# Kernel tuning notes

Measured on AMD Instinct MI355X. Metric: run time of the kernel, lower is better.

The kernel has to match this reference:

```python
import jax, jax.numpy as jnp
import numpy as np

TOPK = 2


def _conv2d(x, w, b):
    # x: (B, Cin, H, W), w: (Cout, Cin, 3, 3), SAME padding (padding=1)
    y = jax.lax.conv_general_dilated(
        x, w, window_strides=(1, 1), padding='SAME',
        dimension_numbers=('NCHW', 'OIHW', 'NCHW'))
    return y + b[None, :, None, None]


def _msunit(x2d, c1w, c1b, c2w, c2b):
    # TimesNet-style 2D unit: conv(1->d_model) -> GELU -> conv(d_model->1)
    h = jax.nn.gelu(_conv2d(x2d, c1w, c1b))
    return _conv2d(h, c2w, c2b)


def setup_inputs():
    B, T, H, DM = 256, 2048, 720, 64
    key = jax.random.key(0)
    ks = jax.random.split(key, 5)
    x = jax.random.normal(ks[0], (B, 1, T), jnp.float32)
    conv1_w = jax.random.normal(ks[1], (DM, 1, 3, 3), jnp.float32) * 0.1
    conv1_b = jnp.zeros((DM,), jnp.float32)
    conv2_w = jax.random.normal(ks[2], (1, DM, 3, 3), jnp.float32) * 0.1
    conv2_b = jnp.zeros((1,), jnp.float32)
    head_w = jax.random.normal(ks[3], (H, T), jnp.float32) * 0.02
    head_b = jnp.zeros((H,), jnp.float32)
    return {'x': x, 'conv1_w': conv1_w, 'conv1_b': conv1_b,
            'conv2_w': conv2_w, 'conv2_b': conv2_b,
            'head_w': head_w, 'head_b': head_b}


def reference(x, conv1_w, conv1_b, conv2_w, conv2_b, head_w, head_b):
    B, _, T = x.shape
    # FFT amplitude spectrum, batch-averaged, drop DC bin
    amp = jnp.abs(jnp.fft.rfft(x[:, 0, :], axis=-1)).mean(0)[1:]
    vals, idx = jax.lax.top_k(amp, TOPK)
    # data-dependent period selection (mirrors .item() calls in torch -> Python ints)
    freqs = np.asarray(idx) + 1
    P_list = [max(1, int(round(T / int(f)))) for f in freqs]
    weights = jax.nn.softmax(vals.astype(x.dtype))
    y = jnp.zeros_like(x)
    for i, P in enumerate(P_list):
        cols = (T + P - 1) // P
        pad = P * cols - T
        xp = jnp.pad(x, ((0, 0), (0, 0), (0, pad)))
        x2d = xp.reshape(B, 1, cols, P).transpose(0, 1, 3, 2)  # (B,1,P,cols)
        y2d = _msunit(x2d, conv1_w, conv1_b, conv2_w, conv2_b)  # (B,1,P,cols)
        y1d = y2d.transpose(0, 1, 3, 2).reshape(B, 1, cols * P)[..., :T]
        y = y + weights[i] * y1d
    out = y[:, 0, :] @ head_w.T + head_b  # (B, horizon)
    return out
```

## Files before the change

### kernel.cpp

```cpp
#include <hip/hip_runtime.h>
#include <math.h>

#define T_LEN   2048
#define NB      256
#define N_FREQ  1024
#define DMODEL  64
#define HORIZON 720

#define WS_META 0
#define WS_AMP  64
#define WS_Y0   2048
#define WS_Y1   (2048 + NB * T_LEN)

#define PMAX_FAST 191
#define CHUNK   1024
#define NCHUNK  2
#define HSTRIDE 1412
#define ZSLOT   1408
#define XSMAX   1824
#define ZXS     (XSMAX - 1)

typedef _Float16 h4 __attribute__((ext_vector_type(4)));
typedef float    fx4 __attribute__((ext_vector_type(4)));

__device__ __forceinline__ float gelu_fast(float a) {
    float a2 = a * a;
    float z  = a * fmaf(-0.07135481627159498f, a2, -1.5957691216057308f);
    float e  = __expf(z);
    return a * __builtin_amdgcn_rcpf(1.0f + e);
}

__device__ __forceinline__ float2 cmul(float2 a, float2 b) {
    return make_float2(a.x * b.x - a.y * b.y, a.x * b.y + a.y * b.x);
}

__device__ __forceinline__ void compute_meta(const float* __restrict__ amp,
                                             float* sf, int* si, int tid,
                                             int& P1, int& cols1, int& P2, int& cols2,
                                             float& wg1, float& wg2) {
    float* v1s = sf;        float* v2s = sf + 256;
    int*   i1s = si;        int*   i2s = si + 256;
    float4 v4 = ((const float4*)amp)[tid];
    float vv[4] = {v4.x, v4.y, v4.z, v4.w};
    float v1 = -1e30f, v2 = -1e30f; int i1 = 1 << 30, i2 = 1 << 30;
    #pragma unroll
    for (int u = 0; u < 4; ++u) {
        int j = tid * 4 + u;
        float v = vv[u];
        if (v > v1) { v2 = v1; i2 = i1; v1 = v; i1 = j; }
        else if (v > v2) { v2 = v; i2 = j; }
    }
    v1s[tid] = v1; i1s[tid] = i1; v2s[tid] = v2; i2s[tid] = i2;
    __syncthreads();
    for (int st = 128; st > 0; st >>= 1) {
        if (tid < st) {
            float w1 = v1s[tid + st]; int j1 = i1s[tid + st];
            float w2 = v2s[tid + st]; int j2 = i2s[tid + st];
            float a1 = v1s[tid];      int a1i = i1s[tid];
            float a2 = v2s[tid];      int a2i = i2s[tid];
            float n1, n2; int n1i, n2i;
            bool w1_first = (w1 > a1) || (w1 == a1 && j1 < a1i);
            if (w1_first) {
                n1 = w1; n1i = j1;
                bool a1_next = (a1 > w2) || (a1 == w2 && a1i < j2);
                if (a1_next) { n2 = a1; n2i = a1i; } else { n2 = w2; n2i = j2; }
            } else {
                n1 = a1; n1i = a1i;
                bool w1_next = (w1 > a2) || (w1 == a2 && j1 < a2i);
                if (w1_next) { n2 = w1; n2i = j1; } else { n2 = a2; n2i = a2i; }
            }
            v1s[tid] = n1; i1s[tid] = n1i; v2s[tid] = n2; i2s[tid] = n2i;
        }
        __syncthreads();
    }
    float v1f = v1s[0], v2f = v2s[0];
    int f1 = i1s[0] + 1, f2 = i2s[0] + 1;
    __syncthreads();
    P1 = (int)llround(2048.0 / (double)f1); if (P1 < 1) P1 = 1;
    P2 = (int)llround(2048.0 / (double)f2); if (P2 < 1) P2 = 1;
    cols1 = (T_LEN + P1 - 1) / P1;
    cols2 = (T_LEN + P2 - 1) / P2;
    float mx = fmaxf(v1f, v2f);
    float e1 = __expf(v1f - mx), e2 = __expf(v2f - mx);
    float inv = 1.0f / (e1 + e2);
    wg1 = e1 * inv; wg2 = e2 * inv;
}

__global__ __launch_bounds__(1024) void fft_amp_kernel(const float* __restrict__ x,
                                                       float* __restrict__ amp) {
    __shared__ float2 buf0[2048];
    __shared__ float2 buf1[2048];
    __shared__ float2 tw[1024];
    const int tid = threadIdx.x;
    const int b = blockIdx.x;

    {
        float s, c;
        __sincosf((float)tid * 3.0679615757712823e-3f, &s, &c);
        tw[tid] = make_float2(c, -s);
    }
    const float* xa = x + (2 * b) * T_LEN;
    const float* xb = x + (2 * b + 1) * T_LEN;
    buf0[tid]        = make_float2(xa[tid],        xb[tid]);
    buf0[tid + 1024] = make_float2(xa[tid + 1024], xb[tid + 1024]);
    __syncthreads();

    float2* src = buf0;
    float2* dst = buf1;
    for (int s = 0; s < 10; s += 2) {
        const int Ns = 1 << s;
        if (tid < 512) {
            const int j1 = tid;
            const int q  = j1 & (Ns - 1);
            const int hi = j1 >> s;
            float2 A = src[j1];
            float2 B = src[j1 + 1024];
            float2 C = src[j1 + 512];
            float2 D = src[j1 + 1536];
            float2 w  = tw[q << (10 - s)];
            float2 wB = cmul(w, B);
            float2 wD = cmul(w, D);
            float2 P0 = make_float2(A.x + wB.x, A.y + wB.y);
            float2 P1 = make_float2(A.x - wB.x, A.y - wB.y);
            float2 Q0 = make_float2(C.x + wD.x, C.y + wD.y);
            float2 Q1 = make_float2(C.x - wD.x, C.y - wD.y);
            float2 wa = tw[q << (9 - s)];
            float2 wb = tw[(q + Ns) << (9 - s)];
            float2 t0 = cmul(wa, Q0);
            float2 t1 = cmul(wb, Q1);
            const int O = (hi << (s + 2)) + q;
            dst[O]          = make_float2(P0.x + t0.x, P0.y + t0.y);
            dst[O + 2 * Ns] = make_float2(P0.x - t0.x, P0.y - t0.y);
            dst[O + Ns]     = make_float2(P1.x + t1.x, P1.y + t1.y);
            dst[O + 3 * Ns] = make_float2(P1.x - t1.x, P1.y - t1.y);
        }
        __syncthreads();
        float2* tmp = src; src = dst; dst = tmp;
    }
    {
        float2 a  = src[tid];
        float2 bb = src[tid + 1024];
        float2 w  = tw[tid];
        float2 t  = cmul(w, bb);
        dst[tid]        = make_float2(a.x + t.x, a.y + t.y);
        dst[tid + 1024] = make_float2(a.x - t.x, a.y - t.y);
        __syncthreads();
        float2* tmp = src; src = dst; dst = tmp;
    }
    const int kk = (tid + b * 8) & 1023;
    const int k = kk + 1;
    float2 Zk = src[k];
    float2 Zn = src[2048 - k];
    float ar = 0.5f * (Zk.x + Zn.x), ai = 0.5f * (Zk.y - Zn.y);
    float br = 0.5f * (Zk.y + Zn.y), bi = 0.5f * (Zk.x - Zn.x);
    float mag = (sqrtf(ar * ar + ai * ai) + sqrtf(br * br + bi * bi)) * (1.0f / 256.0f);
    atomicAdd(amp + kk, mag);
}

__global__ __launch_bounds__(256) void conv_fast_kernel(
    const float* __restrict__ x,
    const float* __restrict__ w1, const float* __restrict__ b1,
    const float* __restrict__ w2, const float* __restrict__ b2,
    const float* __restrict__ amp,
    float* __restrict__ ws, float* __restrict__ out)
{
    __shared__ float xs[XSMAX];
    __shared__ _Float16 dk[9][HSTRIDE];

    const int tid = threadIdx.x;
    {
        const int bid = blockIdx.y * gridDim.x + blockIdx.x;
        if (tid < 45) {
            int idx = bid * 45 + tid;
            if (idx < (NB * HORIZON) / 4)
                ((float4*)out)[idx] = make_float4(0.f, 0.f, 0.f, 0.f);
        }
    }

    int P1, cols1, P2, cols2; float wg1, wg2;
    compute_meta(amp, xs, (int*)(xs + 512), tid, P1, cols1, P2, cols2, wg1, wg2);

    if (blockIdx.x == 0 && blockIdx.y == 0 && tid == 0) {
        int* mi = (int*)ws;
        mi[0] = P1; mi[1] = cols1; mi[2] = P2; mi[3] = cols2;
        ws[4] = wg1; ws[5] = wg2;
    }

    const int per  = blockIdx.y;
    const int P    = per == 0 ? P1 : P2;
    const int cols = per == 0 ? cols1 : cols2;
    if (P > PMAX_FAST) return;
    const float wgt = per == 0 ? wg1 : wg2;
    float* yout = ws + (per == 0 ? WS_Y0 : WS_Y1);

    const int b   = blockIdx.x >> 1;
    const int ci  = blockIdx.x & 1;
    const int t0  = ci * CHUNK;
    const int U0  = t0 - (P + 1);
    const int HN  = CHUNK + 2 * P + 2;
    const int X0  = t0 - (2 * P + 2);
    const int XN  = CHUNK + 4 * P + 4;

    __syncthreads();
    for (int j = tid; j < XSMAX; j += 256) {
        int t = X0 + j;
        xs[j] = (j < XN && t >= 0 && t < T_LEN) ? x[b * T_LEN + t] : 0.f;
    }
    __syncthreads();

    const int lane = tid & 63;
    const int wv   = tid >> 6;
    const int lm   = lane & 15;
    const int lg   = lane >> 4;

    h4  w1f[4], w2f[4];
    fx4 b1f[4];
    #pragma unroll
    for (int t = 0; t < 4; ++t) {
        #pragma unroll
        for (int i = 0; i < 4; ++i) {
            const int k = lg * 4 + i;
            w1f[t][i] = (_Float16)((k < 9) ? w1[(t * 16 + lm) * 9 + k] : 0.f);
            w2f[t][i] = (_Float16)((lm < 9) ? w2[(t * 16 + k) * 9 + lm] : 0.f);
            b1f[t][i] = b1[t * 16 + k];
        }
    }

    const int HN16 = (HN + 15) >> 4;
    const fx4 zf4 = {0.f, 0.f, 0.f, 0.f};

    for (int nt = wv; nt < HN16; nt += 4) {
        const int ih = nt * 16 + lm;
        const int u  = U0 + ih;
        const int uu = u < 0 ? 0 : u;
        const int cc = uu / P;
        const int pp = uu - cc * P;
        const bool rm = pp > 0, rp = pp < P - 1, cm = cc > 0, cp = (cc + 1) < cols;
        const int ibase = ih + P + 1;
        h4 xb;
        #pragma unroll
        for (int j = 0; j < 4; ++j) {
            const int tap = lg * 4 + j;
            const int q = (tap * 86) >> 8;
            const int r = tap - q * 3;
            const bool ok = (tap < 9)
                && (q > 0 || rm) && (q < 2 || rp)
                && (r > 0 || cm) && (r < 2 || cp);
            const int addr = ok ? (ibase + (r - 1) * P + (q - 1)) : ZXS;
            xb[j] = (_Float16)xs[addr];
        }
        fx4 h0 = __builtin_amdgcn_mfma_f32_16x16x16f16(w1f[0], xb, b1f[0], 0, 0, 0);
        fx4 h1 = __builtin_amdgcn_mfma_f32_16x16x16f16(w1f[1], xb, b1f[1], 0, 0, 0);
        fx4 h2 = __builtin_amdgcn_mfma_f32_16x16x16f16(w1f[2], xb, b1f[2], 0, 0, 0);
        fx4 h3 = __builtin_amdgcn_mfma_f32_16x16x16f16(w1f[3], xb, b1f[3], 0, 0, 0);
        h4 g0, g1, g2, g3;
        #pragma unroll
        for (int i = 0; i < 4; ++i) {
            g0[i] = (_Float16)gelu_fast(h0[i]);
            g1[i] = (_Float16)gelu_fast(h1[i]);
            g2[i] = (_Float16)gelu_fast(h2[i]);
            g3[i] = (_Float16)gelu_fast(h3[i]);
        }
        fx4 da = __builtin_amdgcn_mfma_f32_16x16x16f16(w2f[0], g0, zf4, 0, 0, 0);
        fx4 db = __builtin_amdgcn_mfma_f32_16x16x16f16(w2f[1], g1, zf4, 0, 0, 0);
        da = __builtin_amdgcn_mfma_f32_16x16x16f16(w2f[2], g2, da, 0, 0, 0);
        db = __builtin_amdgcn_mfma_f32_16x16x16f16(w2f[3], g3, db, 0, 0, 0);
        if (ih < HN) {
            #pragma unroll
            for (int i = 0; i < 4; ++i) {
                const int row = lg * 4 + i;
                if (row < 9) dk[row][ih] = (_Float16)(da[i] + db[i]);
            }
        }
    }
    if (tid < 9) dk[tid][ZSLOT] = (_Float16)0.f;
    __syncthreads();

    const float bias2 = b2[0];
    #pragma unroll
    for (int o = 0; o < 4; ++o) {
        const int t = t0 + tid + o * 256;
        const int iout = tid + o * 256 + (P + 1);
        const int cc = t / P;
        const int pp = t - cc * P;
        const bool rm = pp > 0, rp = pp < P - 1, cm = cc > 0, cp = (cc + 1) < cols;
        const int i0 = (rm && cm) ? iout - P - 1 : ZSLOT;
        const int i1 = rm         ? iout - 1     : ZSLOT;
        const int i2 = (rm && cp) ? iout + P - 1 : ZSLOT;
        const int i3 = cm         ? iout - P     : ZSLOT;
        const int i5 = cp         ? iout + P     : ZSLOT;
        const int i6 = (rp && cm) ? iout - P + 1 : ZSLOT;
        const int i7 = rp         ? iout + 1     : ZSLOT;
        const int i8 = (rp && cp) ? iout + P + 1 : ZSLOT;
        float s = (float)dk[4][iout];
        s += (float)dk[0][i0]; s += (float)dk[1][i1]; s += (float)dk[2][i2];
        s += (float)dk[3][i3]; s += (float)dk[5][i5]; s += (float)dk[6][i6];
        s += (float)dk[7][i7]; s += (float)dk[8][i8];
        yout[b * T_LEN + t] = wgt * (s + bias2);
    }
}

__global__ __launch_bounds__(256) void conv_unit_kernel(
    const float* __restrict__ x,
    const float* __restrict__ w1, const float* __restrict__ b1,
    const float* __restrict__ w2, const float* __restrict__ b2,
    float* __restrict__ ws)
{
    const int* mi = (const int*)ws;
    const int per   = blockIdx.y;
    const int P     = mi[per * 2 + 0];
    const int cols  = mi[per * 2 + 1];
    if (P <= PMAX_FAST) return;
    const float wgt = ws[4 + per];
    float* yout = ws + (per == 0 ? WS_Y0 : WS_Y1);

    __shared__ float w1s[DMODEL * 9];
    __shared__ float w2s[DMODEL * 9];
    __shared__ float b1s[DMODEL];
    __shared__ float xs[12][13];
    __shared__ float hs[DMODEL][101];

    const int tid = threadIdx.x;
    for (int i = tid; i < DMODEL * 9; i += 256) { w1s[i] = w1[i]; w2s[i] = w2[i]; }
    if (tid < DMODEL) b1s[tid] = b1[tid];
    const float bias2 = b2[0];

    const int tp = (P + 7) >> 3;
    const int tc = (cols + 7) >> 3;
    const int tiles_img = tp * tc;
    const int total = tiles_img * NB;

    for (int tile = blockIdx.x; tile < total; tile += gridDim.x) {
        const int b   = tile / tiles_img;
        const int ti  = tile - b * tiles_img;
        const int tpi = ti / tc;
        const int tci = ti - tpi * tc;
        const int p0 = tpi * 8, c0 = tci * 8;

        __syncthreads();
        if (tid < 144) {
            int i = tid / 12, j = tid - (tid / 12) * 12;
            int pp = p0 - 2 + i, cc = c0 - 2 + j;
            float v = 0.f;
            if (pp >= 0 && pp < P && cc >= 0 && cc < cols) {
                int t = cc * P + pp;
                if (t < T_LEN) v = x[b * T_LEN + t];
            }
            xs[i][j] = v;
        }
        __syncthreads();

        #pragma unroll
        for (int it = 0; it < 25; ++it) {
            int idx = it * 256 + tid;
            int ch = idx / 100;
            int px = idx - ch * 100;
            int pi = px / 10;
            int pj = px - pi * 10;
            const float* w = &w1s[ch * 9];
            float a = b1s[ch];
            a = fmaf(w[0], xs[pi    ][pj    ], a);
            a = fmaf(w[1], xs[pi    ][pj + 1], a);
            a = fmaf(w[2], xs[pi    ][pj + 2], a);
            a = fmaf(w[3], xs[pi + 1][pj    ], a);
            a = fmaf(w[4], xs[pi + 1][pj + 1], a);
            a = fmaf(w[5], xs[pi + 1][pj + 2], a);
            a = fmaf(w[6], xs[pi + 2][pj    ], a);
            a = fmaf(w[7], xs[pi + 2][pj + 1], a);
            a = fmaf(w[8], xs[pi + 2][pj + 2], a);
            float g = gelu_fast(a);
            int pp = p0 - 1 + pi, cc = c0 - 1 + pj;
            bool in_img = (pp >= 0) & (pp < P) & (cc >= 0) & (cc < cols);
            hs[ch][px] = in_img ? g : 0.0f;
        }
        __syncthreads();

        {
            const int pixel = tid >> 2, part = tid & 3;
            const int pi = pixel >> 3, pj = pixel & 7;
            const int base = pi * 10 + pj;
            float s = 0.f;
            for (int ch = part * 16; ch < part * 16 + 16; ++ch) {
                const float* w  = &w2s[ch * 9];
                const float* hr = &hs[ch][base];
                s = fmaf(w[0], hr[0],  s);
                s = fmaf(w[1], hr[1],  s);
                s = fmaf(w[2], hr[2],  s);
                s = fmaf(w[3], hr[10], s);
                s = fmaf(w[4], hr[11], s);
                s = fmaf(w[5], hr[12], s);
                s = fmaf(w[6], hr[20], s);
                s = fmaf(w[7], hr[21], s);
                s = fmaf(w[8], hr[22], s);
            }
            s += __shfl_down(s, 1);
            s += __shfl_down(s, 2);
            if (part == 0) {
                int pp = p0 + pi, cc = c0 + pj;
                if (pp < P && cc < cols) {
                    int t = cc * P + pp;
                    if (t < T_LEN) yout[b * T_LEN + t] = wgt * (s + bias2);
                }
            }
        }
    }
}

__global__ __launch_bounds__(256) void head_gemm_kernel(
    const float* __restrict__ ws, const float* __restrict__ hw,
    const float* __restrict__ hb, float* __restrict__ out)
{
    const float* y0 = ws + WS_Y0;
    const float* y1 = ws + WS_Y1;
    const int b0 = blockIdx.x * 32, h0 = blockIdx.y * 32;
    const int kc0 = blockIdx.z * 512;
    __shared__ float As[32][33];
    __shared__ float Bs[32][33];
    const int tid = threadIdx.x;
    const int tx = tid & 15, ty = tid >> 4;
    const int i0 = ty * 2, j0 = tx * 2;
    const int sr = tid >> 3;
    const int sc = (tid & 7) * 4;
    float a00 = 0.f, a01 = 0.f, a10 = 0.f, a11 = 0.f;
    for (int k0 = kc0; k0 < kc0 + 512; k0 += 32) {
        {
            const int src = (b0 + sr) * T_LEN + k0 + sc;
            float4 u = *(const float4*)(y0 + src);
            float4 v = *(const float4*)(y1 + src);
            As[sr][sc]     = u.x + v.x;
            As[sr][sc + 1] = u.y + v.y;
            As[sr][sc + 2] = u.z + v.z;
            As[sr][sc + 3] = u.w + v.w;
            const int hrow = h0 + sr;
            float4 w = (hrow < HORIZON) ? *(const float4*)(hw + hrow * T_LEN + k0 + sc)
                                        : make_float4(0.f, 0.f, 0.f, 0.f);
            Bs[sr][sc]     = w.x;
            Bs[sr][sc + 1] = w.y;
            Bs[sr][sc + 2] = w.z;
            Bs[sr][sc + 3] = w.w;
        }
        __syncthreads();
        #pragma unroll
        for (int kk = 0; kk < 32; ++kk) {
            float av0 = As[i0][kk], av1 = As[i0 + 1][kk];
            float bv0 = Bs[j0][kk], bv1 = Bs[j0 + 1][kk];
            a00 = fmaf(av0, bv0, a00); a01 = fmaf(av0, bv1, a01);
            a10 = fmaf(av1, bv0, a10); a11 = fmaf(av1, bv1, a11);
        }
        __syncthreads();
    }
    const int bi = b0 + i0, hj = h0 + j0;
    if (blockIdx.z == 0) {
        if (hj < HORIZON)     { float bb = hb[hj];     a00 += bb; a10 += bb; }
        if (hj + 1 < HORIZON) { float bb = hb[hj + 1]; a01 += bb; a11 += bb; }
    }
    if (hj < HORIZON) {
        atomicAdd(&out[bi * HORIZON + hj], a00);
        atomicAdd(&out[(bi + 1) * HORIZON + hj], a10);
    }
    if (hj + 1 < HORIZON) {
        atomicAdd(&out[bi * HORIZON + hj + 1], a01);
        atomicAdd(&out[(bi + 1) * HORIZON + hj + 1], a11);
    }
}

extern "C" void kernel_launch(void* const* d_in, const int* in_sizes, int n_in,
                              void* d_out, int out_size, void* d_ws, size_t ws_size,
                              hipStream_t stream) {
    const float* x   = (const float*)d_in[0];
    const float* c1w = (const float*)d_in[1];
    const float* c1b = (const float*)d_in[2];
    const float* c2w = (const float*)d_in[3];
    const float* c2b = (const float*)d_in[4];
    const float* hw  = (const float*)d_in[5];
    const float* hb  = (const float*)d_in[6];
    float* out = (float*)d_out;
    float* ws  = (float*)d_ws;

    float* amp = ws + WS_AMP;

    hipMemsetAsync(amp, 0, N_FREQ * sizeof(float), stream);
    fft_amp_kernel<<<NB / 2, 1024, 0, stream>>>(x, amp);
    conv_fast_kernel<<<dim3(NB * NCHUNK, 2), 256, 0, stream>>>(x, c1w, c1b, c2w, c2b, amp, ws, out);
    conv_unit_kernel<<<dim3(256, 2), 256, 0, stream>>>(x, c1w, c1b, c2w, c2b, ws);
    head_gemm_kernel<<<dim3(NB / 32, (HORIZON + 31) / 32, 4), 256, 0, stream>>>(ws, hw, hb, out);
}
```

Measured before the change: 152.6 us.

## Use zero-padded column layout in LDS for conv fast path

Replaces the flat 1D input and intermediate buffers with a 2D layout padded by one zero row on each side of every period column (stride P+2). Boundary handling then comes from the padding instead of per-tap predicates and redirects to a zero slot. Input is stored as fp16 in shared memory, and integer division by P is replaced with magic-number multiply-high. The trade-offs are a larger dk buffer, extra zero-fill work for the padding, and periods P<2 being routed to the slow kernel.

```diff
diff --git a/kernel.cpp b/kernel.cpp
--- a/kernel.cpp
+++ b/kernel.cpp
@@ -15,10 +15,9 @@
 #define PMAX_FAST 191
 #define CHUNK   1024
 #define NCHUNK  2
-#define HSTRIDE 1412
-#define ZSLOT   1408
-#define XSMAX   1824
-#define ZXS     (XSMAX - 1)
+
+#define DKSTRIDE 2084
+#define XS2N     2560
 
 typedef _Float16 h4 __attribute__((ext_vector_type(4)));
 typedef float    fx4 __attribute__((ext_vector_type(4)));
@@ -32,6 +31,10 @@
 
 __device__ __forceinline__ float2 cmul(float2 a, float2 b) {
     return make_float2(a.x * b.x - a.y * b.y, a.x * b.y + a.y * b.x);
+}
+
+__device__ __forceinline__ unsigned magic_div(unsigned d) {
+    return (unsigned)((0x100000000ULL + d - 1) / d);
 }
 
 __device__ __forceinline__ void compute_meta(const float* __restrict__ amp,
@@ -164,8 +167,8 @@
     const float* __restrict__ amp,
     float* __restrict__ ws, float* __restrict__ out)
 {
-    __shared__ float xs[XSMAX];
-    __shared__ _Float16 dk[9][HSTRIDE];
+    __shared__ _Float16 xs2[XS2N];
+    __shared__ _Float16 dk[9][DKSTRIDE];
 
     const int tid = threadIdx.x;
     {
@@ -178,7 +181,8 @@
     }
 
     int P1, cols1, P2, cols2; float wg1, wg2;
-    compute_meta(amp, xs, (int*)(xs + 512), tid, P1, cols1, P2, cols2, wg1, wg2);
+    compute_meta(amp, (float*)dk, (int*)(((float*)dk) + 512), tid,
+                 P1, cols1, P2, cols2, wg1, wg2);
 
     if (blockIdx.x == 0 && blockIdx.y == 0 && tid == 0) {
         int* mi = (int*)ws;
@@ -189,22 +193,62 @@
     const int per  = blockIdx.y;
     const int P    = per == 0 ? P1 : P2;
     const int cols = per == 0 ? cols1 : cols2;
-    if (P > PMAX_FAST) return;
+    if (P > PMAX_FAST || P < 2) return;
     const float wgt = per == 0 ? wg1 : wg2;
     float* yout = ws + (per == 0 ? WS_Y0 : WS_Y1);
 
     const int b   = blockIdx.x >> 1;
     const int ci  = blockIdx.x & 1;
     const int t0  = ci * CHUNK;
-    const int U0  = t0 - (P + 1);
-    const int HN  = CHUNK + 2 * P + 2;
-    const int X0  = t0 - (2 * P + 2);
-    const int XN  = CHUNK + 4 * P + 4;
+
+    const int S = P + 2;
+    const unsigned MP = magic_div((unsigned)P);
+    const unsigned MS = magic_div((unsigned)S);
+    const int c_lo = (int)__umulhi((unsigned)t0, MP);
+    const int c_hi = (int)__umulhi((unsigned)(t0 + CHUNK - 1), MP);
+    const int span = c_hi - c_lo;
+    const int LO_hi = span + 3;
+    const int NXC   = span + 7;
+    const int CBASE = 3 - c_lo;
+    const int PBASE = CBASE * S + 1;
+    const int PB2   = PBASE - 2 * S;
+    const int cstart = (c_lo - 1 > 0) ? c_lo - 1 : 0;
+    const int cend_  = (c_hi + 1 < cols - 1) ? c_hi + 1 : cols - 1;
+    const int th0 = cstart * P;
+    const int thN = (cend_ + 1) * P - th0;
+    const bool needL = (c_lo - 1 < 0);
+    const bool needR = (c_hi + 1 > cols - 1);
 
     __syncthreads();
-    for (int j = tid; j < XSMAX; j += 256) {
-        int t = X0 + j;
-        xs[j] = (j < XN && t >= 0 && t < T_LEN) ? x[b * T_LEN + t] : 0.f;
+
+    const int bT = b * T_LEN;
+    for (int j = tid; j < XS2N; j += 256) {
+        int col = (int)__umulhi((unsigned)j, MS);
+        int row = j - col * S;
+        int cc = col - CBASE;
+        int pp = row - 1;
+        int t = cc * P + pp;
+        bool ok = (row >= 1) & (row <= P) & (col >= 1) & (col <= NXC - 2)
+                & (cc >= 0) & (cc < cols) & (t < T_LEN);
+        float v = 0.f;
+        if (ok) v = x[bT + t];
+        xs2[j] = (_Float16)v;
+    }
+    for (int m = tid; m < LO_hi; m += 256) {
+        int base = m * S;
+        #pragma unroll
+        for (int k = 0; k < 9; ++k) { dk[k][base] = (_Float16)0.f; dk[k][base + S - 1] = (_Float16)0.f; }
+    }
+    if (needL) {
+        for (int r = tid; r < S; r += 256)
+            #pragma unroll
+            for (int k = 0; k < 9; ++k) dk[k][r] = (_Float16)0.f;
+    }
+    if (needR) {
+        const int cb = (LO_hi - 1) * S;
+        for (int r = tid; r < S; r += 256)
+            #pragma unroll
+            for (int k = 0; k < 9; ++k) dk[k][cb + r] = (_Float16)0.f;
     }
     __syncthreads();
 
@@ -225,30 +269,29 @@
             b1f[t][i] = b1[t * 16 + k];
         }
     }
-
-    const int HN16 = (HN + 15) >> 4;
+    int eoff[4];
+    #pragma unroll
+    for (int j = 0; j < 4; ++j) {
+        const int ta = lg * 4 + j;
+        const int q = (ta * 86) >> 8;
+        const int r = ta - q * 3;
+        eoff[j] = (ta < 9) ? ((r - 1) * S + (q - 1)) : 0;
+    }
+
+    const int nIter = (thN + 15) >> 4;
     const fx4 zf4 = {0.f, 0.f, 0.f, 0.f};
 
-    for (int nt = wv; nt < HN16; nt += 4) {
-        const int ih = nt * 16 + lm;
-        const int u  = U0 + ih;
-        const int uu = u < 0 ? 0 : u;
-        const int cc = uu / P;
-        const int pp = uu - cc * P;
-        const bool rm = pp > 0, rp = pp < P - 1, cm = cc > 0, cp = (cc + 1) < cols;
-        const int ibase = ih + P + 1;
+    for (int it = wv; it < nIter; it += 4) {
+        const int idx = it * 16 + lm;
+        const int th = th0 + idx;
+        const int cc = (int)__umulhi((unsigned)th, MP);
+        const int pp = th - cc * P;
+        const int pos = cc * S + pp + PBASE;
         h4 xb;
-        #pragma unroll
-        for (int j = 0; j < 4; ++j) {
-            const int tap = lg * 4 + j;
-            const int q = (tap * 86) >> 8;
-            const int r = tap - q * 3;
-            const bool ok = (tap < 9)
-                && (q > 0 || rm) && (q < 2 || rp)
-                && (r > 0 || cm) && (r < 2 || cp);
-            const int addr = ok ? (ibase + (r - 1) * P + (q - 1)) : ZXS;
-            xb[j] = (_Float16)xs[addr];
-        }
+        xb[0] = xs2[pos + eoff[0]];
+        xb[1] = xs2[pos + eoff[1]];
+        xb[2] = xs2[pos + eoff[2]];
+        xb[3] = xs2[pos + eoff[3]];
         fx4 h0 = __builtin_amdgcn_mfma_f32_16x16x16f16(w1f[0], xb, b1f[0], 0, 0, 0);
         fx4 h1 = __builtin_amdgcn_mfma_f32_16x16x16f16(w1f[1], xb, b1f[1], 0, 0, 0);
         fx4 h2 = __builtin_amdgcn_mfma_f32_16x16x16f16(w1f[2], xb, b1f[2], 0, 0, 0);
@@ -265,38 +308,34 @@
         fx4 db = __builtin_amdgcn_mfma_f32_16x16x16f16(w2f[1], g1, zf4, 0, 0, 0);
         da = __builtin_amdgcn_mfma_f32_16x16x16f16(w2f[2], g2, da, 0, 0, 0);
         db = __builtin_amdgcn_mfma_f32_16x16x16f16(w2f[3], g3, db, 0, 0, 0);
-        if (ih < HN) {
+        if (idx < thN) {
+            const int dki = pos - 2 * S;
             #pragma unroll
             for (int i = 0; i < 4; ++i) {
                 const int row = lg * 4 + i;
-                if (row < 9) dk[row][ih] = (_Float16)(da[i] + db[i]);
+                if (row < 9) dk[row][dki] = (_Float16)(da[i] + db[i]);
             }
         }
     }
-    if (tid < 9) dk[tid][ZSLOT] = (_Float16)0.f;
     __syncthreads();
 
     const float bias2 = b2[0];
     #pragma unroll
     for (int o = 0; o < 4; ++o) {
         const int t = t0 + tid + o * 256;
-        const int iout = tid + o * 256 + (P + 1);
-        const int cc = t / P;
+        const int cc = (int)__umulhi((unsigned)t, MP);
         const int pp = t - cc * P;
-        const bool rm = pp > 0, rp = pp < P - 1, cm = cc > 0, cp = (cc + 1) < cols;
-        const int i0 = (rm && cm) ? iout - P - 1 : ZSLOT;
-        const int i1 = rm         ? iout - 1     : ZSLOT;
-        const int i2 = (rm && cp) ? iout + P - 1 : ZSLOT;
-        const int i3 = cm         ? iout - P     : ZSLOT;
-        const int i5 = cp         ? iout + P     : ZSLOT;
-        const int i6 = (rp && cm) ? iout - P + 1 : ZSLOT;
-        const int i7 = rp         ? iout + 1     : ZSLOT;
-        const int i8 = (rp && cp) ? iout + P + 1 : ZSLOT;
-        float s = (float)dk[4][iout];
-        s += (float)dk[0][i0]; s += (float)dk[1][i1]; s += (float)dk[2][i2];
-        s += (float)dk[3][i3]; s += (float)dk[5][i5]; s += (float)dk[6][i6];
-        s += (float)dk[7][i7]; s += (float)dk[8][i8];
-        yout[b * T_LEN + t] = wgt * (s + bias2);
+        const int pd = cc * S + pp + PB2;
+        float s = (float)dk[4][pd];
+        s += (float)dk[0][pd - S - 1];
+        s += (float)dk[1][pd - 1];
+        s += (float)dk[2][pd + S - 1];
+        s += (float)dk[3][pd - S];
+        s += (float)dk[5][pd + S];
+        s += (float)dk[6][pd - S + 1];
+        s += (float)dk[7][pd + 1];
+        s += (float)dk[8][pd + S + 1];
+        yout[bT + t] = wgt * (s + bias2);
     }
 }
 
@@ -310,7 +349,7 @@
     const int per   = blockIdx.y;
     const int P     = mi[per * 2 + 0];
     const int cols  = mi[per * 2 + 1];
-    if (P <= PMAX_FAST) return;
+    if (P <= PMAX_FAST && P >= 2) return;
     const float wgt = ws[4 + per];
     float* yout = ws + (per == 0 ? WS_Y0 : WS_Y1);
 
```

Measured after the change: 157.3 us. 1.03x slower.
